# Kernel tuning notes

Hardware: AMD Instinct MI355X
Metric: run time of the kernel (lower is better)

Reference implementation:

```python
import jax, jax.numpy as jnp
import numpy as np

THETA = 0.5  # forward default arg
ALPHA = 0.2  # LeakyReLU negative slope
NEG_INF = -9e15


def setup_inputs() -> dict:
    key = jax.random.key(0)
    k1, k2, k3, k4, k5 = jax.random.split(key, 5)
    N, F_IN, F_OUT = 8192, 256, 256
    h = jax.random.normal(k1, (N, F_IN), dtype=jnp.float32)
    adj = jax.random.randint(k2, (N, N), 0, 2, dtype=jnp.int32)
    cv_values = jax.random.uniform(k3, (N,), dtype=jnp.float32)
    # xavier_uniform with gain=1.414
    g = 1.414
    bw = g * np.sqrt(6.0 / (F_IN + F_OUT))
    W = jax.random.uniform(k4, (F_IN, F_OUT), dtype=jnp.float32, minval=-bw, maxval=bw)
    ba = g * np.sqrt(6.0 / (2 * F_OUT + 1))
    a = jax.random.uniform(k5, (2 * F_OUT, 1), dtype=jnp.float32, minval=-ba, maxval=ba)
    return {"h": h, "adj": adj, "cv_values": cv_values, "W": W, "a": a}


def reference(h, adj, cv_values, W, a):
    # Wh: [N, F_out]
    Wh = h @ W
    F_out = Wh.shape[1]
    a1 = a[:F_out, 0]   # [F_out]
    a2 = a[F_out:, 0]   # [F_out]
    # e_ij = LeakyReLU([Wh_i ; Wh_j] . a) = LeakyReLU(Wh_i.a1 + Wh_j.a2)
    f1 = Wh @ a1        # [N]
    f2 = Wh @ a2        # [N]
    e = jax.nn.leaky_relu(f1[:, None] + f2[None, :], negative_slope=ALPHA)
    # CV bias: theta * cv_i broadcast across row i
    e = e + THETA * cv_values[:, None]
    att = jnp.where(adj > 0, e, jnp.float32(NEG_INF))
    att = jax.nn.softmax(att, axis=1)
    # dropout is identity in eval mode (training=False)
    h_prime = att @ Wh  # [N, F_out]
    return jax.nn.elu(h_prime)  # concat=True branch
```

## Files before the change

kernel.cpp:

```cpp
#include <hip/hip_runtime.h>
#include <cstdint>
#include <cstddef>

typedef _Float16 half8 __attribute__((ext_vector_type(8)));
typedef _Float16 half4 __attribute__((ext_vector_type(4)));
typedef float f32x4 __attribute__((ext_vector_type(4)));

#define GAT_N 8192
#define GAT_F 256
#define GAT_NW 256
#define GAT_ALPHA 0.2f
#define GAT_LOG2E 1.4426950408889634f

__device__ inline unsigned enc_f32(float x) {
    unsigned b = __float_as_uint(x);
    return (b & 0x80000000u) ? ~b : (b | 0x80000000u);
}
__device__ inline float dec_f32(unsigned u) {
    unsigned b = (u & 0x80000000u) ? (u ^ 0x80000000u) : ~u;
    return __uint_as_float(b);
}

__global__ __launch_bounds__(256) void gat_k0_pack(
    const int* __restrict__ adj, unsigned char* __restrict__ adjB)
{
    const int wv = threadIdx.x >> 6;
    const int lane = threadIdx.x & 63;
    const int row = blockIdx.x * 4 + wv;
    const int* src = adj + (size_t)row * GAT_N;
    unsigned char* dst = adjB + (size_t)row * (GAT_N / 8);
    #pragma unroll 4
    for (int k = 0; k < 16; ++k) {
        const int4 v0 = *reinterpret_cast<const int4*>(src + k * 512 + lane * 8);
        const int4 v1 = *reinterpret_cast<const int4*>(src + k * 512 + lane * 8 + 4);
        unsigned m = (unsigned)(v0.x > 0)        | ((unsigned)(v0.y > 0) << 1)
                   | ((unsigned)(v0.z > 0) << 2) | ((unsigned)(v0.w > 0) << 3)
                   | ((unsigned)(v1.x > 0) << 4) | ((unsigned)(v1.y > 0) << 5)
                   | ((unsigned)(v1.z > 0) << 6) | ((unsigned)(v1.w > 0) << 7);
        dst[k * 64 + lane] = (unsigned char)m;
    }
}

__global__ __launch_bounds__(256) void gat_k0b_convert(
    const float* __restrict__ W, _Float16* __restrict__ WT,
    unsigned* __restrict__ f2mxEnc)
{
    const int g = blockIdx.x * 256 + threadIdx.x;
    if (g == 0) *f2mxEnc = 0u;
    const int k = g >> 8, n = g & 255;
    WT[n * GAT_F + k] = (_Float16)W[g];
}

__global__ __launch_bounds__(256, 2) void gat_k1_gemm(
    const float* __restrict__ h, const _Float16* __restrict__ WT,
    const float* __restrict__ a, _Float16* __restrict__ whT,
    float* __restrict__ f1L, float* __restrict__ f2L,
    unsigned* __restrict__ f2mxEnc)
{
    __shared__ float sP1[4][16], sP2[4][16];
    const int wv = threadIdx.x >> 6;
    const int lane = threadIdx.x & 63;
    const int l15 = lane & 15;
    const int quad = lane >> 4;
    const int r0 = blockIdx.x * 16;

    f32x4 acc[4];
    #pragma unroll
    for (int t = 0; t < 4; ++t) { f32x4 z = {0.f,0.f,0.f,0.f}; acc[t] = z; }

    #pragma unroll
    for (int k0 = 0; k0 < GAT_F; k0 += 32) {
        const float* ap = h + (size_t)(r0 + l15) * GAT_F + k0 + quad * 8;
        const float4 a0 = *reinterpret_cast<const float4*>(ap);
        const float4 a1 = *reinterpret_cast<const float4*>(ap + 4);
        half8 af;
        af[0] = (_Float16)a0.x; af[1] = (_Float16)a0.y;
        af[2] = (_Float16)a0.z; af[3] = (_Float16)a0.w;
        af[4] = (_Float16)a1.x; af[5] = (_Float16)a1.y;
        af[6] = (_Float16)a1.z; af[7] = (_Float16)a1.w;
        #pragma unroll
        for (int t = 0; t < 4; ++t) {
            half8 bf = *reinterpret_cast<const half8*>(
                WT + (size_t)(wv * 64 + t * 16 + l15) * GAT_F + k0 + quad * 8);
            acc[t] = __builtin_amdgcn_mfma_f32_16x16x32_f16(af, bf, acc[t], 0, 0, 0);
        }
    }

    float p1[4] = {0.f,0.f,0.f,0.f}, p2[4] = {0.f,0.f,0.f,0.f};
    #pragma unroll
    for (int t = 0; t < 4; ++t) {
        float a1c = a[wv * 64 + t * 16 + l15];
        float a2c = a[GAT_F + wv * 64 + t * 16 + l15];
        #pragma unroll
        for (int r = 0; r < 4; ++r) {
            p1[r] = fmaf(acc[t][r], a1c, p1[r]);
            p2[r] = fmaf(acc[t][r], a2c, p2[r]);
        }
    }
    #pragma unroll
    for (int off = 1; off < 16; off <<= 1) {
        #pragma unroll
        for (int r = 0; r < 4; ++r) {
            p1[r] += __shfl_xor(p1[r], off);
            p2[r] += __shfl_xor(p2[r], off);
        }
    }
    if (l15 == 0) {
        #pragma unroll
        for (int r = 0; r < 4; ++r) {
            sP1[wv][quad * 4 + r] = p1[r];
            sP2[wv][quad * 4 + r] = p2[r];
        }
    }
    __syncthreads();
    if (threadIdx.x < 16) {
        const int row = threadIdx.x;
        const float s1 = (sP1[0][row] + sP1[1][row] + sP1[2][row] + sP1[3][row]) * GAT_LOG2E;
        const float s2 = (sP2[0][row] + sP2[1][row] + sP2[2][row] + sP2[3][row]) * GAT_LOG2E;
        f1L[r0 + row] = s1;
        f2L[r0 + row] = s2;
        float mx = s2;
        #pragma unroll
        for (int off = 1; off < 16; off <<= 1) mx = fmaxf(mx, __shfl_xor(mx, off));
        if (row == 0) atomicMax(f2mxEnc, enc_f32(mx));
    }

    #pragma unroll
    for (int t = 0; t < 4; ++t) {
        half4 hv;
        #pragma unroll
        for (int r = 0; r < 4; ++r) hv[r] = (_Float16)acc[t][r];
        *reinterpret_cast<half4*>(
            whT + (size_t)(wv * 64 + t * 16 + l15) * GAT_N + r0 + quad * 4) = hv;
    }
}

__global__ __launch_bounds__(256, 2) void gat_k3_attn(
    const unsigned* __restrict__ adjW, const float* __restrict__ f1L,
    const float* __restrict__ f2L, const unsigned* __restrict__ f2mxEnc,
    const _Float16* __restrict__ whT,
    _Float16* __restrict__ Ph,
    float* __restrict__ L)
{
    __shared__ __align__(16) _Float16 sB[2][16384];

    const int bx = blockIdx.x;
    const int rb = bx >> 3;
    const int q  = bx & 7;
    const int wv = threadIdx.x >> 6;
    const int lane = threadIdx.x & 63;
    const int l15 = lane & 15;
    const int quad = lane >> 4;

    const int r0 = rb * 128 + wv * 32;
    const int rA = r0 + l15;
    const int rB = rA + 16;

    const float fmxL = dec_f32(*f2mxEnc);
    const float f1A = f1L[rA];
    const float f1B = f1L[rB];
    const float sA = f1A + fmxL;
    const float sBv = f1B + fmxL;
    const float CA = fmaxf(sA, GAT_ALPHA * sA);
    const float CB = fmaxf(sBv, GAT_ALPHA * sBv);

    f32x4 acc[2][16];
    #pragma unroll
    for (int s = 0; s < 2; ++s)
        #pragma unroll
        for (int t = 0; t < 16; ++t) {
            f32x4 z = {0.f,0.f,0.f,0.f};
            acc[s][t] = z;
        }
    float d0 = 0.f, d1 = 0.f;

    const int kq = q * 1024;
    const uint4* awA = reinterpret_cast<const uint4*>(adjW + (size_t)rA * GAT_NW + q * 32);
    const uint4* awB = reinterpret_cast<const uint4*>(adjW + (size_t)rB * GAT_NW + q * 32);
    const float* f2q = f2L + kq + quad * 8;

    const _Float16* gst = whT + (size_t)lane * GAT_N + kq + wv * 8;

    #define STAGE(buf, step)                                                   \
        {                                                                      \
            _Pragma("unroll")                                                  \
            for (int i = 0; i < 8; ++i) {                                      \
                const _Float16* gp = gst + (size_t)((i & 3) * 64) * GAT_N      \
                                     + (i >> 2) * 32 + (step) * 64;            \
                _Float16* lp = &sB[buf][(((wv + (i >> 2) * 4) * 256            \
                                          + (i & 3) * 64)) * 8];               \
                __builtin_amdgcn_global_load_lds(                              \
                    (const __attribute__((address_space(1))) void*)gp,         \
                    (__attribute__((address_space(3))) void*)lp, 16, 0, 0);    \
            }                                                                  \
        }

    uint4 nA = awA[0];
    uint4 nB = awB[0];
    float4 nfa = *reinterpret_cast<const float4*>(f2q);
    float4 nfb = *reinterpret_cast<const float4*>(f2q + 4);
    STAGE(0, 0)
    __syncthreads();

    for (int grp = 0; grp < 8; ++grp) {
        const uint4 cA = nA, cB = nB;
        if (grp < 7) { nA = awA[grp + 1]; nB = awB[grp + 1]; }

        #pragma unroll
        for (int s = 0; s < 2; ++s) {
            const int step = grp * 2 + s;
            const int cur = step & 1;
            if (step + 1 < 16) STAGE(1 - cur, step + 1)

            #pragma unroll
            for (int k2 = 0; k2 < 2; ++k2) {
                const int u = step * 2 + k2;
                const float4 cfa = nfa, cfb = nfb;
                if (u < 31) {
                    nfa = *reinterpret_cast<const float4*>(f2q + (u + 1) * 32);
                    nfb = *reinterpret_cast<const float4*>(f2q + (u + 1) * 32 + 4);
                }
                const int wi = s * 2 + k2;
                const unsigned wA = (wi == 0) ? cA.x : (wi == 1) ? cA.y
                                  : (wi == 2) ? cA.z : cA.w;
                const unsigned wB = (wi == 0) ? cB.x : (wi == 1) ? cB.y
                                  : (wi == 2) ? cB.z : cB.w;
                const unsigned mA = (wA >> (quad * 8)) & 0xffu;
                const unsigned mB = (wB >> (quad * 8)) & 0xffu;
                const float f2v[8] = {cfa.x, cfa.y, cfa.z, cfa.w,
                                      cfb.x, cfb.y, cfb.z, cfb.w};

                half8 pA, pB;
                #pragma unroll
                for (int j = 0; j < 8; ++j) {
                    const float f2j = f2v[j];
                    float xa = f1A + f2j;
                    float la = fmaxf(xa, GAT_ALPHA * xa);
                    float pa = __builtin_amdgcn_exp2f(la - CA);
                    pa = (mA & (1u << j)) ? pa : 0.f;
                    d0 += pa;
                    pA[j] = (_Float16)pa;
                    float xb = f1B + f2j;
                    float lb = fmaxf(xb, GAT_ALPHA * xb);
                    float pb = __builtin_amdgcn_exp2f(lb - CB);
                    pb = (mB & (1u << j)) ? pb : 0.f;
                    d1 += pb;
                    pB[j] = (_Float16)pb;
                }

                const int lbase = (k2 * 1024 + quad * 256 + l15) * 8;
                #pragma unroll
                for (int t = 0; t < 16; ++t) {
                    half8 bf = *reinterpret_cast<const half8*>(
                        &sB[cur][lbase + t * 128]);
                    acc[0][t] = __builtin_amdgcn_mfma_f32_16x16x32_f16(pA, bf, acc[0][t], 0, 0, 0);
                    acc[1][t] = __builtin_amdgcn_mfma_f32_16x16x32_f16(pB, bf, acc[1][t], 0, 0, 0);
                }
            }
            __syncthreads();
        }
    }
    #undef STAGE

    d0 += __shfl_xor(d0, 16); d0 += __shfl_xor(d0, 32);
    d1 += __shfl_xor(d1, 16); d1 += __shfl_xor(d1, 32);
    float* Lq = L + q * GAT_N;
    if (lane < 16) { Lq[rA] = d0; Lq[rB] = d1; }

    const int wid = rb * 4 + wv;
    _Float16* Pq = Ph + ((size_t)q * 256 + wid) * 8192;
    #pragma unroll
    for (int s = 0; s < 2; ++s)
        #pragma unroll
        for (int t = 0; t < 16; ++t) {
            half4 hv;
            #pragma unroll
            for (int r = 0; r < 4; ++r) hv[r] = (_Float16)acc[s][t][r];
            *reinterpret_cast<half4*>(Pq + (size_t)(((s * 16 + t) * 64 + lane) * 4)) = hv;
        }
}

__global__ __launch_bounds__(256) void gat_k4_final(
    const _Float16* __restrict__ Ph, const float* __restrict__ L,
    float* __restrict__ out)
{
    const int tid = threadIdx.x;
    const int wid = blockIdx.x >> 3;
    __shared__ float s_rl[32];
    if (tid < 32) {
        const int row = wid * 32 + tid;
        float s = 0.f;
        #pragma unroll
        for (int q = 0; q < 8; ++q) s += L[q * GAT_N + row];
        s_rl[tid] = 1.0f / fmaxf(s, 1e-30f);
    }
    __syncthreads();

    const int idx = blockIdx.x * 256 + tid;
    const int rem = idx & 2047;
    const int lane = rem & 63;
    const int st = rem >> 6;
    const int s = st >> 4, t = st & 15;
    const int l15 = lane & 15, quad = lane >> 4;
    const int lrow0 = s * 16 + quad * 4;
    const int col = t * 16 + l15;

    float accv[4] = {0.f, 0.f, 0.f, 0.f};
    #pragma unroll
    for (int q = 0; q < 8; ++q) {
        half4 v = *reinterpret_cast<const half4*>(
            Ph + ((size_t)q * 256 + wid) * 8192 + (size_t)rem * 4);
        #pragma unroll
        for (int r = 0; r < 4; ++r) accv[r] += (float)v[r];
    }
    #pragma unroll
    for (int r = 0; r < 4; ++r) {
        const float v = accv[r] * s_rl[lrow0 + r];
        const float o = v > 0.f ? v : expm1f(v);
        out[(size_t)(wid * 32 + lrow0 + r) * GAT_F + col] = o;
    }
}

extern "C" void kernel_launch(void* const* d_in, const int* in_sizes, int n_in,
                              void* d_out, int out_size, void* d_ws, size_t ws_size,
                              hipStream_t stream)
{
    const float* h   = (const float*)d_in[0];
    const int*   adj = (const int*)d_in[1];
    const float* W   = (const float*)d_in[3];
    const float* a   = (const float*)d_in[4];
    float* out = (float*)d_out;
    char* ws = (char*)d_ws;

    const size_t SLAB = (size_t)GAT_N * GAT_F * 2;

    size_t off = 0;
    _Float16* whT = (_Float16*)(ws + off); off += SLAB;
    _Float16* Ph  = (_Float16*)(ws + off); off += 8 * SLAB;
    unsigned char* adjB = (unsigned char*)(ws + off); off += (size_t)GAT_N * GAT_N / 8;
    _Float16* WT  = (_Float16*)(ws + off); off += (size_t)GAT_F * GAT_F * 2;
    float* f1L = (float*)(ws + off); off += GAT_N * 4;
    float* f2L = (float*)(ws + off); off += GAT_N * 4;
    float* L   = (float*)(ws + off); off += 8 * GAT_N * 4;
    unsigned* f2mxEnc = (unsigned*)(ws + off); off += 256;

    gat_k0_pack<<<2048, 256, 0, stream>>>(adj, adjB);
    gat_k0b_convert<<<256, 256, 0, stream>>>(W, WT, f2mxEnc);
    gat_k1_gemm<<<512, 256, 0, stream>>>(h, WT, a, whT, f1L, f2L, f2mxEnc);
    gat_k3_attn<<<512, 256, 0, stream>>>((const unsigned*)adjB, f1L, f2L, f2mxEnc, whT, Ph, L);
    gat_k4_final<<<2048, 256, 0, stream>>>(Ph, L, out);
}
```

Measured before the change: 483.5 us.

## Split attention kernel across two feature halves to double grid and occupancy

Result: faster. 466.5 us (-3.5%).

```diff
diff --git a/kernel.cpp b/kernel.cpp
--- a/kernel.cpp
+++ b/kernel.cpp
@@ -135,18 +135,19 @@
     }
 }
 
-__global__ __launch_bounds__(256, 2) void gat_k3_attn(
+__global__ __launch_bounds__(256, 3) void gat_k3_attn(
     const unsigned* __restrict__ adjW, const float* __restrict__ f1L,
     const float* __restrict__ f2L, const unsigned* __restrict__ f2mxEnc,
     const _Float16* __restrict__ whT,
     _Float16* __restrict__ Ph,
     float* __restrict__ L)
 {
-    __shared__ __align__(16) _Float16 sB[2][16384];
+    __shared__ __align__(16) _Float16 sB[2][8192];
 
     const int bx = blockIdx.x;
-    const int rb = bx >> 3;
     const int q  = bx & 7;
+    const int fh = (bx >> 3) & 1;
+    const int rb = bx >> 4;
     const int wv = threadIdx.x >> 6;
     const int lane = threadIdx.x & 63;
     const int l15 = lane & 15;
@@ -164,119 +165,117 @@
     const float CA = fmaxf(sA, GAT_ALPHA * sA);
     const float CB = fmaxf(sBv, GAT_ALPHA * sBv);
 
-    f32x4 acc[2][16];
+    f32x4 acc[2][8];
     #pragma unroll
     for (int s = 0; s < 2; ++s)
         #pragma unroll
-        for (int t = 0; t < 16; ++t) {
+        for (int t = 0; t < 8; ++t) {
             f32x4 z = {0.f,0.f,0.f,0.f};
             acc[s][t] = z;
         }
     float d0 = 0.f, d1 = 0.f;
 
     const int kq = q * 1024;
-    const uint4* awA = reinterpret_cast<const uint4*>(adjW + (size_t)rA * GAT_NW + q * 32);
-    const uint4* awB = reinterpret_cast<const uint4*>(adjW + (size_t)rB * GAT_NW + q * 32);
+    const uint2* awA = reinterpret_cast<const uint2*>(adjW + (size_t)rA * GAT_NW + q * 32);
+    const uint2* awB = reinterpret_cast<const uint2*>(adjW + (size_t)rB * GAT_NW + q * 32);
     const float* f2q = f2L + kq + quad * 8;
 
-    const _Float16* gst = whT + (size_t)lane * GAT_N + kq + wv * 8;
+    const _Float16* gst = whT + (size_t)(fh * 128 + lane) * GAT_N + kq + wv * 8;
 
     #define STAGE(buf, step)                                                   \
         {                                                                      \
             _Pragma("unroll")                                                  \
-            for (int i = 0; i < 8; ++i) {                                      \
-                const _Float16* gp = gst + (size_t)((i & 3) * 64) * GAT_N      \
-                                     + (i >> 2) * 32 + (step) * 64;            \
-                _Float16* lp = &sB[buf][(((wv + (i >> 2) * 4) * 256            \
-                                          + (i & 3) * 64)) * 8];               \
+            for (int i = 0; i < 4; ++i) {                                      \
+                const _Float16* gp = gst + (size_t)((i & 1) * 64) * GAT_N      \
+                                     + (i >> 1) * 32 + (step) * 64;            \
+                _Float16* lp = &sB[buf][((wv + (i >> 1) * 4) * 128             \
+                                         + (i & 1) * 64) * 8];                 \
                 __builtin_amdgcn_global_load_lds(                              \
                     (const __attribute__((address_space(1))) void*)gp,         \
                     (__attribute__((address_space(3))) void*)lp, 16, 0, 0);    \
             }                                                                  \
         }
 
-    uint4 nA = awA[0];
-    uint4 nB = awB[0];
+    uint2 nA = awA[0];
+    uint2 nB = awB[0];
     float4 nfa = *reinterpret_cast<const float4*>(f2q);
     float4 nfb = *reinterpret_cast<const float4*>(f2q + 4);
     STAGE(0, 0)
     __syncthreads();
 
-    for (int grp = 0; grp < 8; ++grp) {
-        const uint4 cA = nA, cB = nB;
-        if (grp < 7) { nA = awA[grp + 1]; nB = awB[grp + 1]; }
-
-        #pragma unroll
-        for (int s = 0; s < 2; ++s) {
-            const int step = grp * 2 + s;
-            const int cur = step & 1;
-            if (step + 1 < 16) STAGE(1 - cur, step + 1)
-
+    for (int step = 0; step < 16; ++step) {
+        const int cur = step & 1;
+        const uint2 cA = nA, cB = nB;
+        if (step < 15) {
+            nA = awA[step + 1];
+            nB = awB[step + 1];
+            STAGE(1 - cur, step + 1)
+        }
+
+        #pragma unroll
+        for (int k2 = 0; k2 < 2; ++k2) {
+            const int u = step * 2 + k2;
+            const float4 cfa = nfa, cfb = nfb;
+            if (u < 31) {
+                nfa = *reinterpret_cast<const float4*>(f2q + (u + 1) * 32);
+                nfb = *reinterpret_cast<const float4*>(f2q + (u + 1) * 32 + 4);
+            }
+            const unsigned wA = k2 ? cA.y : cA.x;
+            const unsigned wB = k2 ? cB.y : cB.x;
+            const unsigned mA = (wA >> (quad * 8)) & 0xffu;
+            const unsigned mB = (wB >> (quad * 8)) & 0xffu;
+            const float f2v[8] = {cfa.x, cfa.y, cfa.z, cfa.w,
+                                  cfb.x, cfb.y, cfb.z, cfb.w};
+
+            half8 pA, pB;
             #pragma unroll
-            for (int k2 = 0; k2 < 2; ++k2) {
-                const int u = step * 2 + k2;
-                const float4 cfa = nfa, cfb = nfb;
-                if (u < 31) {
-                    nfa = *reinterpret_cast<const float4*>(f2q + (u + 1) * 32);
-                    nfb = *reinterpret_cast<const float4*>(f2q + (u + 1) * 32 + 4);
-                }
-                const int wi = s * 2 + k2;
-                const unsigned wA = (wi == 0) ? cA.x : (wi == 1) ? cA.y
-                                  : (wi == 2) ? cA.z : cA.w;
-                const unsigned wB = (wi == 0) ? cB.x : (wi == 1) ? cB.y
-                                  : (wi == 2) ? cB.z : cB.w;
-                const unsigned mA = (wA >> (quad * 8)) & 0xffu;
-                const unsigned mB = (wB >> (quad * 8)) & 0xffu;
-                const float f2v[8] = {cfa.x, cfa.y, cfa.z, cfa.w,
-                                      cfb.x, cfb.y, cfb.z, cfb.w};
-
-                half8 pA, pB;
-                #pragma unroll
-                for (int j = 0; j < 8; ++j) {
-                    const float f2j = f2v[j];
-                    float xa = f1A + f2j;
-                    float la = fmaxf(xa, GAT_ALPHA * xa);
-                    float pa = __builtin_amdgcn_exp2f(la - CA);
-                    pa = (mA & (1u << j)) ? pa : 0.f;
-                    d0 += pa;
-                    pA[j] = (_Float16)pa;
-                    float xb = f1B + f2j;
-                    float lb = fmaxf(xb, GAT_ALPHA * xb);
-                    float pb = __builtin_amdgcn_exp2f(lb - CB);
-                    pb = (mB & (1u << j)) ? pb : 0.f;
-                    d1 += pb;
-                    pB[j] = (_Float16)pb;
-                }
-
-                const int lbase = (k2 * 1024 + quad * 256 + l15) * 8;
-                #pragma unroll
-                for (int t = 0; t < 16; ++t) {
-                    half8 bf = *reinterpret_cast<const half8*>(
-                        &sB[cur][lbase + t * 128]);
-                    acc[0][t] = __builtin_amdgcn_mfma_f32_16x16x32_f16(pA, bf, acc[0][t], 0, 0, 0);
-                    acc[1][t] = __builtin_amdgcn_mfma_f32_16x16x32_f16(pB, bf, acc[1][t], 0, 0, 0);
-                }
+            for (int j = 0; j < 8; ++j) {
+                const float f2j = f2v[j];
+                float xa = f1A + f2j;
+                float la = fmaxf(xa, GAT_ALPHA * xa);
+                float pa = __builtin_amdgcn_exp2f(la - CA);
+                pa = (mA & (1u << j)) ? pa : 0.f;
+                d0 += pa;
+                pA[j] = (_Float16)pa;
+                float xb = f1B + f2j;
+                float lb = fmaxf(xb, GAT_ALPHA * xb);
+                float pb = __builtin_amdgcn_exp2f(lb - CB);
+                pb = (mB & (1u << j)) ? pb : 0.f;
+                d1 += pb;
+                pB[j] = (_Float16)pb;
             }
-            __syncthreads();
-        }
+
+            const int lbase = (k2 * 4 + quad) * 1024 + l15 * 8;
+            #pragma unroll
+            for (int t = 0; t < 8; ++t) {
+                half8 bf = *reinterpret_cast<const half8*>(
+                    &sB[cur][lbase + t * 128]);
+                acc[0][t] = __builtin_amdgcn_mfma_f32_16x16x32_f16(pA, bf, acc[0][t], 0, 0, 0);
+                acc[1][t] = __builtin_amdgcn_mfma_f32_16x16x32_f16(pB, bf, acc[1][t], 0, 0, 0);
+            }
+        }
+        __syncthreads();
     }
     #undef STAGE
 
     d0 += __shfl_xor(d0, 16); d0 += __shfl_xor(d0, 32);
     d1 += __shfl_xor(d1, 16); d1 += __shfl_xor(d1, 32);
-    float* Lq = L + q * GAT_N;
-    if (lane < 16) { Lq[rA] = d0; Lq[rB] = d1; }
+    if (fh == 0 && lane < 16) {
+        float* Lq = L + q * GAT_N;
+        Lq[rA] = d0; Lq[rB] = d1;
+    }
 
     const int wid = rb * 4 + wv;
     _Float16* Pq = Ph + ((size_t)q * 256 + wid) * 8192;
     #pragma unroll
     for (int s = 0; s < 2; ++s)
         #pragma unroll
-        for (int t = 0; t < 16; ++t) {
+        for (int t = 0; t < 8; ++t) {
+            const int tt = fh * 8 + t;
             half4 hv;
             #pragma unroll
             for (int r = 0; r < 4; ++r) hv[r] = (_Float16)acc[s][t][r];
-            *reinterpret_cast<half4*>(Pq + (size_t)(((s * 16 + t) * 64 + lane) * 4)) = hv;
+            *reinterpret_cast<half4*>(Pq + (size_t)(((s * 16 + tt) * 64 + lane) * 4)) = hv;
         }
 }
 
@@ -347,6 +346,6 @@
     gat_k0_pack<<<2048, 256, 0, stream>>>(adj, adjB);
     gat_k0b_convert<<<256, 256, 0, stream>>>(W, WT, f2mxEnc);
     gat_k1_gemm<<<512, 256, 0, stream>>>(h, WT, a, whT, f1L, f2L, f2mxEnc);
-    gat_k3_attn<<<512, 256, 0, stream>>>((const unsigned*)adjB, f1L, f2L, f2mxEnc, whT, Ph, L);
+    gat_k3_attn<<<1024, 256, 0, stream>>>((const unsigned*)adjB, f1L, f2L, f2mxEnc, whT, Ph, L);
     gat_k4_final<<<2048, 256, 0, stream>>>(Ph, L, out);
 }
```
